# Kernel tuning notes

Measured on AMD Instinct MI355X. Metric: run time of the kernel, lower is better.

The kernel has to match this reference:

```python
import jax, jax.numpy as jnp
import numpy as np

C = 256; C_OUT = 256; HD = 32; NH = 8; WS = 8; SHIFT = WS // 2
B = 2; H = 256; W = 256
HW = H // WS; WW = W // WS; NWIN = HW * WW; P = WS * WS
SCALE = HD ** -0.5
GN_GROUPS = 16; GN_EPS = 1e-5
UP = C // 2; LOW = C - UP; SQ = 2

# relative position index (static)
_ci = np.arange(WS)
_coords = np.stack(np.meshgrid(_ci, _ci, indexing='ij'), -1).reshape(-1, 2)  # [P,2]
_rel = _coords[:, None] - _coords[None, :] + WS - 1                          # [P,P,2]
REL0 = jnp.asarray(_rel[..., 0]); REL1 = jnp.asarray(_rel[..., 1])

# shifted-window mask (static), type != 'W'
_s = WS - SHIFT
_m = np.zeros((HW, WW, WS, WS, WS, WS), bool)
_m[-1, :, :_s, :, _s:, :] = True
_m[-1, :, _s:, :, :_s, :] = True
_m[:, -1, :, :_s, :, _s:] = True
_m[:, -1, :, _s:, :, :_s] = True
MASK = jnp.asarray(_m.reshape(NWIN, P, P))


def to_windows(x):  # [B,H,W,C] -> [B,NWIN,P,C]
    b, h, w, c = x.shape
    return x.reshape(b, h // WS, WS, w // WS, WS, c).transpose(0, 1, 3, 2, 4, 5).reshape(b, NWIN, P, c)


def to_spatial(x):  # [B,NWIN,P,C] -> [B,H,W,C]
    b, _, _, c = x.shape
    return x.reshape(b, HW, WW, WS, WS, c).transpose(0, 1, 3, 2, 4, 5).reshape(b, H, W, c)


def heads(x):  # [B,NWIN,P,C] -> [NH,B,NWIN,P,HD]
    b = x.shape[0]
    return x.reshape(b, NWIN, P, NH, HD).transpose(3, 0, 1, 2, 4)


def conv(x, w, b=None, groups=1, pad=0):
    y = jax.lax.conv_general_dilated(x, w, (1, 1), [(pad, pad), (pad, pad)],
                                     dimension_numbers=('NCHW', 'OIHW', 'NCHW'),
                                     feature_group_count=groups)
    return y if b is None else y + b[None, :, None, None]


def group_norm(x, w, b):  # torch nn.GroupNorm semantics (biased var)
    n, c, h, ww_ = x.shape
    xg = x.reshape(n, GN_GROUPS, -1)
    mu = xg.mean(-1, keepdims=True)
    var = ((xg - mu) ** 2).mean(-1, keepdims=True)
    xg = (xg - mu) / jnp.sqrt(var + GN_EPS)
    return xg.reshape(n, c, h, ww_) * w[None, :, None, None] + b[None, :, None, None]


def sru(x, gn_w, gn_b):
    gn_x = group_norm(x, gn_w, gn_b)
    w_gamma = (gn_w / jnp.sum(gn_w))[None, :, None, None]
    rw = jax.nn.sigmoid(gn_x * w_gamma)
    w1 = jnp.where(rw > 0.5, jnp.ones_like(rw), rw)
    w2 = jnp.where(rw > 0.5, jnp.zeros_like(rw), rw)
    x1 = w1 * x; x2 = w2 * x
    c = x.shape[1] // 2
    return jnp.concatenate([x1[:, :c] + x2[:, c:], x1[:, c:] + x2[:, :c]], axis=1)


def cru(x, sq1_w, sq2_w, gwc_w, gwc_b, pwc1_w, pwc2_w):
    up, low = x[:, :UP], x[:, UP:]
    up = conv(up, sq1_w)          # [B,UP//SQ,H,W]
    low = conv(low, sq2_w)        # [B,LOW//SQ,H,W]
    y1 = conv(up, gwc_w, gwc_b, groups=2, pad=1) + conv(up, pwc1_w)  # [B,C,H,W]
    y2 = jnp.concatenate([conv(low, pwc2_w), low], axis=1)           # [B,C,H,W]
    out = jnp.concatenate([y1, y2], axis=1)                          # [B,2C,H,W]
    pooled = out.mean(axis=(2, 3), keepdims=True)
    out = jax.nn.softmax(pooled, axis=1) * out
    c = out.shape[1] // 2
    return out[:, :c] + out[:, c:]


def setup_inputs():
    key = jax.random.key(0)
    ks = jax.random.split(key, 14)
    r = lambda k, s, sc=1.0: jax.random.normal(k, s, jnp.float32) * sc
    return {
        'x': r(ks[0], (B, C, H, W)),
        'w_qkv': r(ks[1], (3 * C, C), 0.02), 'b_qkv': jnp.zeros((3 * C,), jnp.float32),
        'rel_pos': r(ks[2], (NH, 2 * WS - 1, 2 * WS - 1), 0.02),
        'gn_w': jax.random.uniform(ks[3], (C,), jnp.float32, 0.5, 1.5),
        'gn_b': r(ks[4], (C,), 0.02),
        'sq1_w': r(ks[5], (UP // SQ, UP, 1, 1), 0.05),
        'sq2_w': r(ks[6], (LOW // SQ, LOW, 1, 1), 0.05),
        'gwc_w': r(ks[7], (C, (UP // SQ) // 2, 3, 3), 0.05), 'gwc_b': jnp.zeros((C,), jnp.float32),
        'pwc1_w': r(ks[8], (C, UP // SQ, 1, 1), 0.05),
        'pwc2_w': r(ks[9], (C - LOW // SQ, LOW // SQ, 1, 1), 0.05),
        'w_out': r(ks[10], (C_OUT, C), 0.02), 'b_out': jnp.zeros((C_OUT,), jnp.float32),
    }


def reference(x, w_qkv, b_qkv, rel_pos, gn_w, gn_b, sq1_w, sq2_w, gwc_w, gwc_b, pwc1_w, pwc2_w, w_out, b_out):
    xh = jnp.transpose(x, (0, 2, 3, 1))                       # b h w c
    xh = jnp.roll(xh, (-SHIFT, -SHIFT), axis=(1, 2))          # cyclic shift (type='SW')
    xw = to_windows(xh)                                       # [B,NWIN,P,C]
    qkv = xw @ w_qkv.T + b_qkv                                # [B,NWIN,P,3C]
    # q path: back to spatial -> SRU -> back to windows/heads
    q_sp = jnp.transpose(to_spatial(qkv[..., :C]), (0, 3, 1, 2))
    q_sp = sru(q_sp, gn_w, gn_b)
    q = heads(to_windows(jnp.transpose(q_sp, (0, 2, 3, 1))))  # [NH,B,NWIN,P,HD]
    # k path: CRU
    k_sp = jnp.transpose(to_spatial(qkv[..., C:2 * C]), (0, 3, 1, 2))
    k_sp = cru(k_sp, sq1_w, sq2_w, gwc_w, gwc_b, pwc1_w, pwc2_w)
    k = heads(to_windows(jnp.transpose(k_sp, (0, 2, 3, 1))))
    v = heads(qkv[..., 2 * C:])
    sim = jnp.einsum('hbwpc,hbwqc->hbwpq', q, k) * SCALE
    sim = sim + rel_pos[:, REL0, REL1][:, None, None]         # relative position bias [NH,P,P]
    sim = jnp.where(MASK[None, None], -jnp.inf, sim)
    probs = jax.nn.softmax(sim, axis=-1)
    out = jnp.einsum('hbwpq,hbwqc->hbwpc', probs, v)          # [NH,B,NWIN,P,HD]
    out = jnp.transpose(out, (1, 2, 3, 0, 4)).reshape(B, NWIN, P, C)
    out = out @ w_out.T + b_out
    out = to_spatial(out)                                     # b h w c
    out = jnp.roll(out, (SHIFT, SHIFT), axis=(1, 2))
    return jnp.transpose(out, (0, 3, 1, 2))                   # b c h w
```

## Files before the change

kernel.cpp:

```cpp
#include <hip/hip_runtime.h>
#include <hip/hip_bf16.h>

typedef __hip_bfloat16 bf16;
typedef __attribute__((ext_vector_type(8))) short s16x8;
typedef __attribute__((ext_vector_type(4))) float f32x4;

#define SCALE 0.17677669529663687f

#define OFF_QKV   0ull
#define OFF_UL    201326592ull
#define OFF_CRU   268435456ull
#define OFF_XT    OFF_CRU
#define OFF_POOL  402653184ull
#define OFF_GNACC 402657280ull
#define OFF_GNFIN 402657536ull
#define OFF_SOFT  402658048ull
#define OFF_WC    402662144ull
#define OFF_WC2   403022592ull
#define OFF_WQS   403088128ull
#define OFF_WOS   403481344ull
#define OFF_ATTN  OFF_UL

__device__ __forceinline__ float b2f(bf16 v){ return __bfloat162float(v); }
__device__ __forceinline__ bf16  f2b(float v){ return __float2bfloat16(v); }
__device__ __forceinline__ ushort f2bu(float v){ bf16 b = __float2bfloat16(v); return *(ushort*)&b; }
__device__ __forceinline__ uint pk2(float a, float b){ return (uint)f2bu(a) | ((uint)f2bu(b) << 16); }

__device__ __forceinline__ void gload16(const void* g, void* l){
  __builtin_amdgcn_global_load_lds((const __attribute__((address_space(1))) unsigned int*)g,
                                   (__attribute__((address_space(3))) unsigned int*)l, 16, 0, 0);
}

__global__ void k_wprep(const float* __restrict__ gwc_w, const float* __restrict__ pwc1,
                        const float* __restrict__ pwc2, const float* __restrict__ w_qkv,
                        const float* __restrict__ w_out, float* __restrict__ Wc,
                        float* __restrict__ Wc2, char* __restrict__ wqs, char* __restrict__ wos)
{
  int idx = blockIdx.x * 256 + threadIdx.x;
  if (idx < 90112){
    int c = idx & 127;
    int gk = idx >> 7;
    int g = gk / 352, k = gk - g * 352;
    int ch = g * 128 + c;
    Wc[idx] = (k < 288) ? gwc_w[(size_t)ch * 288 + k] : pwc1[ch * 64 + (k - 288)];
  } else if (idx < 106496){
    int j = idx - 90112;
    int k = j >> 8, c = j & 255;
    Wc2[j] = (c < 192) ? pwc2[c * 64 + k] : (k == (c - 192) ? 1.f : 0.f);
  } else if (idx < 303104){
    int j = idx - 106496;
    int n = j >> 8, k = j & 255;
    *(ushort*)(wqs + (size_t)n * 512 + ((k * 2) ^ ((n & 7) << 4))) = f2bu(w_qkv[n * 256 + k]);
  } else if (idx < 368640){
    int j = idx - 303104;
    int n = j >> 8, k = j & 255;
    *(ushort*)(wos + (size_t)n * 512 + ((k * 2) ^ ((n & 7) << 4))) = f2bu(w_out[n * 256 + k]);
  }
}

__global__ __launch_bounds__(256) void k_xt(const float* __restrict__ x, char* __restrict__ xt)
{
  __shared__ ushort Ls[64][66];
  int t = threadIdx.x;
  int jt = blockIdx.x;
  int i  = blockIdx.y;
  int zc = blockIdx.z;
  int ct = zc & 3, b = zc >> 2;
  int ch0 = ct * 64, j0 = jt * 64;
  for (int e = t; e < 4096; e += 256){
    int ch = e >> 6, jj = e & 63;
    Ls[ch][jj] = f2bu(x[(((size_t)(b * 256 + ch0 + ch)) << 16) + (i << 8) + j0 + jj]);
  }
  __syncthreads();
  int ri = (i - 4) & 255;
  #pragma unroll
  for (int s = 0; s < 2; s++){
    int id = s * 256 + t;
    int jj = id >> 3, blk = id & 7;
    int rj = (j0 + jj - 4) & 255;
    int m = (b << 16) + (ri << 8) + rj;
    ushort u0 = Ls[blk*8+0][jj], u1 = Ls[blk*8+1][jj], u2 = Ls[blk*8+2][jj], u3 = Ls[blk*8+3][jj];
    ushort u4 = Ls[blk*8+4][jj], u5 = Ls[blk*8+5][jj], u6 = Ls[blk*8+6][jj], u7 = Ls[blk*8+7][jj];
    uint4 pkv;
    pkv.x = (uint)u0 | ((uint)u1 << 16);
    pkv.y = (uint)u2 | ((uint)u3 << 16);
    pkv.z = (uint)u4 | ((uint)u5 << 16);
    pkv.w = (uint)u6 | ((uint)u7 << 16);
    size_t byte = (size_t)m * 512 + (((ch0 + blk * 8) * 2) ^ ((m & 7) << 4));
    *(uint4*)(xt + byte) = pkv;
  }
}

__global__ __launch_bounds__(256) void k_qkv_mfma(
    const char* __restrict__ xt, const char* __restrict__ wq,
    const float* __restrict__ bias, bf16* __restrict__ qkv)
{
  __shared__ char sm[32768];
  int t = threadIdx.x;
  int l = t & 63, w = t >> 6;
  int ln = l & 15, l4 = l >> 4;
  int m0 = blockIdx.x * 128, n0 = blockIdx.y * 128;
  int wm0 = (w >> 1) * 64, wn0 = (w & 1) * 64;
  f32x4 acc[4][4];
  #pragma unroll
  for (int a = 0; a < 4; a++)
    #pragma unroll
    for (int c = 0; c < 4; c++) acc[a][c] = (f32x4){0.f, 0.f, 0.f, 0.f};
  const char* gA = xt + (size_t)(m0 + w * 32 + (l >> 3)) * 512 + (l & 7) * 16;
  const char* gB = wq + (size_t)(n0 + w * 32 + (l >> 3)) * 512 + (l & 7) * 16;
  char* ldsA = sm + (w * 32) * 128;
  char* ldsB = sm + 16384 + (w * 32) * 128;
  for (int k0 = 0; k0 < 256; k0 += 64){
    #pragma unroll
    for (int c = 0; c < 4; c++){
      gload16(gA + (size_t)k0 * 2 + c * 4096, ldsA + c * 1024);
      gload16(gB + (size_t)k0 * 2 + c * 4096, ldsB + c * 1024);
    }
    __syncthreads();
    s16x8 af[4][2], bfr[4][2];
    #pragma unroll
    for (int mi = 0; mi < 4; mi++){
      int r = wm0 + mi * 16 + ln;
      int key = (r & 7) << 4;
      #pragma unroll
      for (int kk = 0; kk < 2; kk++)
        af[mi][kk] = *(const s16x8*)(sm + r * 128 + ((kk * 64 + l4 * 16) ^ key));
    }
    #pragma unroll
    for (int ni = 0; ni < 4; ni++){
      int r = wn0 + ni * 16 + ln;
      int key = (r & 7) << 4;
      #pragma unroll
      for (int kk = 0; kk < 2; kk++)
        bfr[ni][kk] = *(const s16x8*)(sm + 16384 + r * 128 + ((kk * 64 + l4 * 16) ^ key));
    }
    #pragma unroll
    for (int kk = 0; kk < 2; kk++)
      #pragma unroll
      for (int mi = 0; mi < 4; mi++)
        #pragma unroll
        for (int ni = 0; ni < 4; ni++)
          acc[mi][ni] = __builtin_amdgcn_mfma_f32_16x16x32_bf16(af[mi][kk], bfr[ni][kk], acc[mi][ni], 0, 0, 0);
    __syncthreads();
  }
  #pragma unroll
  for (int ni = 0; ni < 4; ni++){
    int n = n0 + wn0 + ni * 16 + ln;
    float bs = bias[n];
    #pragma unroll
    for (int mi = 0; mi < 4; mi++){
      int mb = m0 + wm0 + mi * 16 + l4 * 4;
      int b = mb >> 16, pix = mb & 65535;
      ushort4 pkv;
      pkv.x = f2bu(acc[mi][ni].x + bs);
      pkv.y = f2bu(acc[mi][ni].y + bs);
      pkv.z = f2bu(acc[mi][ni].z + bs);
      pkv.w = f2bu(acc[mi][ni].w + bs);
      *(ushort4*)((char*)qkv + (((size_t)(b * 768 + n)) << 17) + pix * 2) = pkv;
    }
  }
}

__global__ __launch_bounds__(256) void k_gn_stats(const bf16* __restrict__ qkv,
                                                  float* __restrict__ acc)
{
  int blk = blockIdx.x;
  int s = blk & 7, bg = blk >> 3;
  int g = bg & 15, b = bg >> 4;
  int t = threadIdx.x;
  float sum = 0.f, sq = 0.f;
  for (int ch = 0; ch < 16; ch++){
    const bf16* base = qkv + (((size_t)(b * 768 + g * 16 + ch)) << 16) + s * 8192;
    for (int p = t; p < 8192; p += 256){
      float v = b2f(base[p]);
      sum += v; sq += v * v;
    }
  }
  __shared__ float rs[256], rq[256];
  rs[t] = sum; rq[t] = sq; __syncthreads();
  for (int st = 128; st > 0; st >>= 1){
    if (t < st){ rs[t] += rs[t + st]; rq[t] += rq[t + st]; }
    __syncthreads();
  }
  if (t == 0){
    atomicAdd(&acc[bg * 2], rs[0]);
    atomicAdd(&acc[bg * 2 + 1], rq[0]);
  }
}

__global__ __launch_bounds__(256) void k_gn_final(const float* __restrict__ acc,
                                                  const float* __restrict__ gn_w,
                                                  float* __restrict__ fin)
{
  __shared__ float red[256];
  int t = threadIdx.x;
  red[t] = gn_w[t]; __syncthreads();
  for (int st = 128; st > 0; st >>= 1){
    if (t < st) red[t] += red[t + st];
    __syncthreads();
  }
  if (t == 0) fin[64] = 1.0f / red[0];
  if (t < 32){
    const float Ninv = 1.0f / 1048576.0f;
    float mu = acc[t * 2] * Ninv;
    float var = acc[t * 2 + 1] * Ninv - mu * mu;
    fin[t * 2] = mu;
    fin[t * 2 + 1] = 1.0f / sqrtf(var + 1e-5f);
  }
}

__global__ __launch_bounds__(256) void k_sru(bf16* __restrict__ qkv,
    const float* __restrict__ fin, const float* __restrict__ gn_w,
    const float* __restrict__ gn_b)
{
  int idx = blockIdx.x * 256 + threadIdx.x;
  int pix = idx & 65535;
  int bc = idx >> 16;
  int c = bc & 127, b = bc >> 7;
  size_t i1 = (((size_t)(b * 768 + c)) << 16) + pix;
  size_t i2 = (((size_t)(b * 768 + c + 128)) << 16) + pix;
  float x1 = b2f(qkv[i1]);
  float x2 = b2f(qkv[i2]);
  int g1 = c >> 4, g2 = (c + 128) >> 4;
  float mu1 = fin[(b * 16 + g1) * 2], rs1 = fin[(b * 16 + g1) * 2 + 1];
  float mu2 = fin[(b * 16 + g2) * 2], rs2 = fin[(b * 16 + g2) * 2 + 1];
  float invs = fin[64];
  float w1c = gn_w[c], w2c = gn_w[c + 128];
  float gnx1 = (x1 - mu1) * rs1 * w1c + gn_b[c];
  float gnx2 = (x2 - mu2) * rs2 * w2c + gn_b[c + 128];
  float rw1 = 1.0f / (1.0f + __expf(-gnx1 * (w1c * invs)));
  float rw2 = 1.0f / (1.0f + __expf(-gnx2 * (w2c * invs)));
  float a1 = rw1 > 0.5f ? 1.0f : rw1, a2 = rw1 > 0.5f ? 0.0f : rw1;
  float b1 = rw2 > 0.5f ? 1.0f : rw2, b2v = rw2 > 0.5f ? 0.0f : rw2;
  qkv[i1] = f2b(a1 * x1 + b2v * x2);
  qkv[i2] = f2b(b1 * x2 + a2 * x1);
}

__global__ __launch_bounds__(256) void k_squeeze(const bf16* __restrict__ qkv,
    const float* __restrict__ sq1, const float* __restrict__ sq2,
    float* __restrict__ ul)
{
  __shared__ float in_s[128][65];
  int p0 = blockIdx.x * 64;
  int b = p0 >> 16, pl0 = p0 & 65535;
  int t = threadIdx.x;
  int pp = t & 63, og = t >> 6;
  for (int e = t; e < 8192; e += 256){
    int ch = e >> 6, px = e & 63;
    in_s[ch][px] = b2f(qkv[(((size_t)(b * 768 + 256 + ch)) << 16) + pl0 + px]);
  }
  __syncthreads();
  {
    float acc[16] = {};
    for (int i = 0; i < 128; i++){
      float v = in_s[i][pp];
      #pragma unroll
      for (int o = 0; o < 16; o++) acc[o] += sq1[(og * 16 + o) * 128 + i] * v;
    }
    #pragma unroll
    for (int o = 0; o < 16; o++)
      ul[(((size_t)(b * 128 + og * 16 + o)) << 16) + pl0 + pp] = acc[o];
  }
  __syncthreads();
  for (int e = t; e < 8192; e += 256){
    int ch = e >> 6, px = e & 63;
    in_s[ch][px] = b2f(qkv[(((size_t)(b * 768 + 384 + ch)) << 16) + pl0 + px]);
  }
  __syncthreads();
  {
    float acc[16] = {};
    for (int i = 0; i < 128; i++){
      float v = in_s[i][pp];
      #pragma unroll
      for (int o = 0; o < 16; o++) acc[o] += sq2[(og * 16 + o) * 128 + i] * v;
    }
    #pragma unroll
    for (int o = 0; o < 16; o++)
      ul[(((size_t)(b * 128 + 64 + og * 16 + o)) << 16) + pl0 + pp] = acc[o];
  }
}

__global__ __launch_bounds__(256) void k_cru_gemm(
    const float* __restrict__ ul, const float* __restrict__ Wmat,
    const float* __restrict__ gwc_b, bf16* __restrict__ cru, int mode)
{
  __shared__ float As[16][132];
  __shared__ float Bs[16][132];
  int t = threadIdx.x;
  int tx = t & 15, ty = t >> 4;
  int tile = blockIdx.x;
  int yT = blockIdx.y;
  int b = blockIdx.z;
  int tr = tile >> 4, tc = tile & 15;
  int ty0 = tr * 8, tx0 = tc * 16;
  int K = (mode == 0) ? 352 : 64;
  const float* W = (mode == 0) ? (Wmat + yT * 352 * 128) : Wmat;
  int wstride = (mode == 0) ? 128 : 256;
  int wcol0 = (mode == 0) ? 0 : yT * 128;
  float acc[8][8] = {};
  for (int k0 = 0; k0 < K; k0 += 16){
    #pragma unroll
    for (int l = 0; l < 8; l++){
      int e = t + l * 256;
      int mm = e & 127, kk = e >> 7;
      int k = k0 + kk;
      int py = mm >> 4, pxx = mm & 15;
      float v;
      if (mode == 0){
        int i, dy, dx;
        if (k < 288){
          i = k / 9; int r9 = k - i * 9; dy = r9 / 3; dx = r9 - dy * 3;
          i += yT * 32;
        } else { i = k - 288; dy = 1; dx = 1; }
        int gy = ty0 + py + dy - 1, gx = tx0 + pxx + dx - 1;
        v = (gy >= 0 && gy < 256 && gx >= 0 && gx < 256)
              ? ul[(((size_t)(b * 128 + i)) << 16) + (gy << 8) + gx] : 0.f;
      } else {
        v = ul[(((size_t)(b * 128 + 64 + k)) << 16) + ((ty0 + py) << 8) + tx0 + pxx];
      }
      As[kk][mm] = v;
    }
    #pragma unroll
    for (int l = 0; l < 8; l++){
      int e = t + l * 256;
      int nn = e & 127, kk = e >> 7;
      Bs[kk][nn] = W[(size_t)(k0 + kk) * wstride + wcol0 + nn];
    }
    __syncthreads();
    #pragma unroll
    for (int kk = 0; kk < 16; kk++){
      float4 a0 = *(const float4*)&As[kk][ty * 4];
      float4 a1 = *(const float4*)&As[kk][64 + ty * 4];
      float4 b0 = *(const float4*)&Bs[kk][tx * 4];
      float4 b1 = *(const float4*)&Bs[kk][64 + tx * 4];
      float av[8] = {a0.x,a0.y,a0.z,a0.w,a1.x,a1.y,a1.z,a1.w};
      float bv[8] = {b0.x,b0.y,b0.z,b0.w,b1.x,b1.y,b1.z,b1.w};
      #pragma unroll
      for (int r = 0; r < 8; r++)
        #pragma unroll
        for (int c = 0; c < 8; c++) acc[r][c] += av[r] * bv[c];
    }
    __syncthreads();
  }
  #pragma unroll
  for (int r = 0; r < 8; r++){
    int mr = (r < 4) ? (ty * 4 + r) : (64 + ty * 4 + r - 4);
    int py = mr >> 4, pxx = mr & 15;
    int gpix = ((ty0 + py) << 8) + tx0 + pxx;
    #pragma unroll
    for (int c = 0; c < 8; c++){
      int nc = (c < 4) ? (tx * 4 + c) : (64 + tx * 4 + c - 4);
      int ch; float bv;
      if (mode == 0){ ch = yT * 128 + nc; bv = gwc_b[ch]; }
      else          { ch = 256 + yT * 128 + nc; bv = 0.f; }
      cru[(((size_t)(b * 512 + ch)) << 16) + gpix] = f2b(acc[r][c] + bv);
    }
  }
}

__global__ __launch_bounds__(256) void k_pool(const bf16* __restrict__ cru,
                                              float* __restrict__ pool)
{
  int bc = blockIdx.x;
  const ushort4* p4 = (const ushort4*)(cru + (((size_t)bc) << 16));
  int t = threadIdx.x;
  float s = 0.f;
  for (int i = t; i < 16384; i += 256){
    ushort4 u = p4[i];
    s += b2f(*(bf16*)&u.x) + b2f(*(bf16*)&u.y) + b2f(*(bf16*)&u.z) + b2f(*(bf16*)&u.w);
  }
  __shared__ float red[256];
  red[t] = s; __syncthreads();
  for (int st = 128; st > 0; st >>= 1){
    if (t < st) red[t] += red[t + st];
    __syncthreads();
  }
  if (t == 0) pool[bc] = red[0];
}

__global__ __launch_bounds__(512) void k_pool_softmax(const float* __restrict__ pool,
                                                      float* __restrict__ s)
{
  __shared__ float red[512];
  int t = threadIdx.x;
  for (int b = 0; b < 2; b++){
    float v = pool[b * 512 + t] * (1.0f / 65536.0f);
    red[t] = v; __syncthreads();
    for (int st = 256; st > 0; st >>= 1){
      if (t < st) red[t] = fmaxf(red[t], red[t + st]);
      __syncthreads();
    }
    float m = red[0]; __syncthreads();
    float e = __expf(v - m);
    red[t] = e; __syncthreads();
    for (int st = 256; st > 0; st >>= 1){
      if (t < st) red[t] += red[t + st];
      __syncthreads();
    }
    float inv = 1.0f / red[0];
    __syncthreads();
    s[b * 512 + t] = e * inv;
  }
}

__global__ __launch_bounds__(256) void k_cru_apply(const bf16* __restrict__ cru,
    const float* __restrict__ s, bf16* __restrict__ qkv)
{
  int idx = blockIdx.x * 256 + threadIdx.x;
  int pix = idx & 65535;
  int bc = idx >> 16;
  int c = bc & 255, b = bc >> 8;
  float v1 = b2f(cru[(((size_t)(b * 512 + c)) << 16) + pix]);
  float v2 = b2f(cru[(((size_t)(b * 512 + 256 + c)) << 16) + pix]);
  float kv = s[b * 512 + c] * v1 + s[b * 512 + 256 + c] * v2;
  qkv[(((size_t)(b * 768 + 256 + c)) << 16) + pix] = f2b(kv);
}

__global__ __launch_bounds__(64) void k_attn(const bf16* __restrict__ qkv,
    const float* __restrict__ rel_pos, char* __restrict__ attnb)
{
  __shared__ float k_s[64][33];
  __shared__ float v_s[64][33];
  __shared__ float bias_s[225];
  int win = blockIdx.x, head = blockIdx.y, b = blockIdx.z;
  int hw = win >> 5, wwi = win & 31;
  int t = threadIdx.x;
  for (int e = t; e < 225; e += 64) bias_s[e] = rel_pos[head * 225 + e];
  int pi = t >> 3, pj = t & 7;
  int pix = ((hw * 8 + pi) << 8) | (wwi * 8 + pj);
  size_t base = ((size_t)(b * 768)) << 16;
  float q[32];
  #pragma unroll
  for (int d = 0; d < 32; d++){
    q[d]      = b2f(qkv[base + (((size_t)(      head * 32 + d)) << 16) + pix]);
    k_s[t][d] = b2f(qkv[base + (((size_t)(256 + head * 32 + d)) << 16) + pix]);
    v_s[t][d] = b2f(qkv[base + (((size_t)(512 + head * 32 + d)) << 16) + pix]);
  }
  __syncthreads();
  bool mH = (hw == 31), mW = (wwi == 31);
  float sim[64];
  float mx = -1e30f;
  #pragma unroll
  for (int j = 0; j < 64; j++){
    float sv = 0.f;
    #pragma unroll
    for (int d = 0; d < 32; d++) sv += q[d] * k_s[j][d];
    int ji = j >> 3, jj = j & 7;
    sv = sv * SCALE + bias_s[(pi - ji + 7) * 15 + (pj - jj + 7)];
    bool masked = (mH && ((pi < 4) != (ji < 4))) || (mW && ((pj < 4) != (jj < 4)));
    sv = masked ? -1e30f : sv;
    sim[j] = sv;
    mx = fmaxf(mx, sv);
  }
  float sum = 0.f;
  #pragma unroll
  for (int j = 0; j < 64; j++){
    float e = __expf(sim[j] - mx);
    sim[j] = e; sum += e;
  }
  float inv = 1.0f / sum;
  float o[32] = {};
  #pragma unroll
  for (int j = 0; j < 64; j++){
    float p = sim[j] * inv;
    #pragma unroll
    for (int d = 0; d < 32; d++) o[d] += p * v_s[j][d];
  }
  int ii = hw * 8 + pi, jjp = wwi * 8 + pj;
  int om = (b << 16) + (((ii + 4) & 255) << 8) + ((jjp + 4) & 255);
  size_t rb = (size_t)om * 512;
  int key = (om & 7) << 4;
  #pragma unroll
  for (int d0 = 0; d0 < 32; d0 += 8){
    uint4 pkv;
    pkv.x = pk2(o[d0+0], o[d0+1]);
    pkv.y = pk2(o[d0+2], o[d0+3]);
    pkv.z = pk2(o[d0+4], o[d0+5]);
    pkv.w = pk2(o[d0+6], o[d0+7]);
    *(uint4*)(attnb + rb + ((head * 64 + d0 * 2) ^ key)) = pkv;
  }
}

__global__ __launch_bounds__(256) void k_proj_mfma(
    const char* __restrict__ at, const char* __restrict__ wo,
    const float* __restrict__ bias, float* __restrict__ outp)
{
  __shared__ char sm[32768];
  int t = threadIdx.x;
  int l = t & 63, w = t >> 6;
  int ln = l & 15, l4 = l >> 4;
  int m0 = blockIdx.x * 128, n0 = blockIdx.y * 128;
  int wm0 = (w >> 1) * 64, wn0 = (w & 1) * 64;
  f32x4 acc[4][4];
  #pragma unroll
  for (int a = 0; a < 4; a++)
    #pragma unroll
    for (int c = 0; c < 4; c++) acc[a][c] = (f32x4){0.f, 0.f, 0.f, 0.f};
  const char* gA = at + (size_t)(m0 + w * 32 + (l >> 3)) * 512 + (l & 7) * 16;
  const char* gB = wo + (size_t)(n0 + w * 32 + (l >> 3)) * 512 + (l & 7) * 16;
  char* ldsA = sm + (w * 32) * 128;
  char* ldsB = sm + 16384 + (w * 32) * 128;
  for (int k0 = 0; k0 < 256; k0 += 64){
    #pragma unroll
    for (int c = 0; c < 4; c++){
      gload16(gA + (size_t)k0 * 2 + c * 4096, ldsA + c * 1024);
      gload16(gB + (size_t)k0 * 2 + c * 4096, ldsB + c * 1024);
    }
    __syncthreads();
    s16x8 af[4][2], bfr[4][2];
    #pragma unroll
    for (int mi = 0; mi < 4; mi++){
      int r = wm0 + mi * 16 + ln;
      int key = (r & 7) << 4;
      #pragma unroll
      for (int kk = 0; kk < 2; kk++)
        af[mi][kk] = *(const s16x8*)(sm + r * 128 + ((kk * 64 + l4 * 16) ^ key));
    }
    #pragma unroll
    for (int ni = 0; ni < 4; ni++){
      int r = wn0 + ni * 16 + ln;
      int key = (r & 7) << 4;
      #pragma unroll
      for (int kk = 0; kk < 2; kk++)
        bfr[ni][kk] = *(const s16x8*)(sm + 16384 + r * 128 + ((kk * 64 + l4 * 16) ^ key));
    }
    #pragma unroll
    for (int kk = 0; kk < 2; kk++)
      #pragma unroll
      for (int mi = 0; mi < 4; mi++)
        #pragma unroll
        for (int ni = 0; ni < 4; ni++)
          acc[mi][ni] = __builtin_amdgcn_mfma_f32_16x16x32_bf16(af[mi][kk], bfr[ni][kk], acc[mi][ni], 0, 0, 0);
    __syncthreads();
  }
  #pragma unroll
  for (int ni = 0; ni < 4; ni++){
    int n = n0 + wn0 + ni * 16 + ln;
    float bs = bias[n];
    #pragma unroll
    for (int mi = 0; mi < 4; mi++){
      int mb = m0 + wm0 + mi * 16 + l4 * 4;
      int b = mb >> 16, pix = mb & 65535;
      float4 v;
      v.x = acc[mi][ni].x + bs;
      v.y = acc[mi][ni].y + bs;
      v.z = acc[mi][ni].z + bs;
      v.w = acc[mi][ni].w + bs;
      *(float4*)(outp + (((size_t)(b * 256 + n)) << 16) + pix) = v;
    }
  }
}

extern "C" void kernel_launch(void* const* d_in, const int* in_sizes, int n_in,
                              void* d_out, int out_size, void* d_ws, size_t ws_size,
                              hipStream_t stream) {
  const float* x       = (const float*)d_in[0];
  const float* w_qkv   = (const float*)d_in[1];
  const float* b_qkv   = (const float*)d_in[2];
  const float* rel_pos = (const float*)d_in[3];
  const float* gn_w    = (const float*)d_in[4];
  const float* gn_b    = (const float*)d_in[5];
  const float* sq1     = (const float*)d_in[6];
  const float* sq2     = (const float*)d_in[7];
  const float* gwc_w   = (const float*)d_in[8];
  const float* gwc_b   = (const float*)d_in[9];
  const float* pwc1    = (const float*)d_in[10];
  const float* pwc2    = (const float*)d_in[11];
  const float* w_out   = (const float*)d_in[12];
  const float* b_out   = (const float*)d_in[13];
  float* out = (float*)d_out;

  char* ws = (char*)d_ws;
  bf16*  qkv   = (bf16*)(ws + OFF_QKV);
  float* ul    = (float*)(ws + OFF_UL);
  bf16*  cru   = (bf16*)(ws + OFF_CRU);
  char*  xt    = ws + OFF_XT;
  float* pool  = (float*)(ws + OFF_POOL);
  float* gnacc = (float*)(ws + OFF_GNACC);
  float* gnfin = (float*)(ws + OFF_GNFIN);
  float* smax  = (float*)(ws + OFF_SOFT);
  float* Wc    = (float*)(ws + OFF_WC);
  float* Wc2   = (float*)(ws + OFF_WC2);
  char*  wqs   = ws + OFF_WQS;
  char*  wos   = ws + OFF_WOS;
  char*  attnb = ws + OFF_ATTN;

  hipMemsetAsync(ws + OFF_GNACC, 0, 256, stream);
  k_wprep<<<1440, 256, 0, stream>>>(gwc_w, pwc1, pwc2, w_qkv, w_out, Wc, Wc2, wqs, wos);
  k_xt<<<dim3(4, 256, 8), 256, 0, stream>>>(x, xt);
  k_qkv_mfma<<<dim3(1024, 6), 256, 0, stream>>>(xt, wqs, b_qkv, qkv);
  k_gn_stats<<<256, 256, 0, stream>>>(qkv, gnacc);
  k_gn_final<<<1, 256, 0, stream>>>(gnacc, gn_w, gnfin);
  k_sru<<<65536, 256, 0, stream>>>(qkv, gnfin, gn_w, gn_b);
  k_squeeze<<<2048, 256, 0, stream>>>(qkv, sq1, sq2, ul);
  k_cru_gemm<<<dim3(512, 2, 2), 256, 0, stream>>>(ul, Wc, gwc_b, cru, 0);
  k_cru_gemm<<<dim3(512, 2, 2), 256, 0, stream>>>(ul, Wc2, gwc_b, cru, 1);
  k_pool<<<1024, 256, 0, stream>>>(cru, pool);
  k_pool_softmax<<<1, 512, 0, stream>>>(pool, smax);
  k_cru_apply<<<131072, 256, 0, stream>>>(cru, smax, qkv);
  k_attn<<<dim3(1024, 8, 2), 64, 0, stream>>>(qkv, rel_pos, attnb);
  k_proj_mfma<<<dim3(1024, 2), 256, 0, stream>>>(attnb, wos, b_out, out);
}
```

Baseline: 2.529 ms.

## Process four adjacent windows per attention block for coalesced loads and reused LDS

The attention kernel now runs 256-thread blocks that each cover four horizontally adjacent windows, so a wavefront reads 32 contiguous pixels per channel plane instead of 8. This gives better-coalesced global loads. K and V share a single float4-vectorized LDS buffer, with V loaded after the softmax, which lowers LDS use and permits three blocks per CU under the launch bounds. The cost is an extra barrier, partial unrolling of the inner loops, and more register pressure.

```diff
diff --git a/kernel.cpp b/kernel.cpp
--- a/kernel.cpp
+++ b/kernel.cpp
@@ -416,58 +416,95 @@
   qkv[(((size_t)(b * 768 + 256 + c)) << 16) + pix] = f2b(kv);
 }
 
-__global__ __launch_bounds__(64) void k_attn(const bf16* __restrict__ qkv,
+__global__ __launch_bounds__(256, 3) void k_attn(const bf16* __restrict__ qkv,
     const float* __restrict__ rel_pos, char* __restrict__ attnb)
 {
-  __shared__ float k_s[64][33];
-  __shared__ float v_s[64][33];
+  __shared__ float kv_s[64 * 4 * 36];
   __shared__ float bias_s[225];
-  int win = blockIdx.x, head = blockIdx.y, b = blockIdx.z;
-  int hw = win >> 5, wwi = win & 31;
-  int t = threadIdx.x;
-  for (int e = t; e < 225; e += 64) bias_s[e] = rel_pos[head * 225 + e];
-  int pi = t >> 3, pj = t & 7;
-  int pix = ((hw * 8 + pi) << 8) | (wwi * 8 + pj);
+  int t = threadIdx.x;
+  int wg = blockIdx.x, hw = blockIdx.y;
+  int z = blockIdx.z;
+  int head = z & 7, b = z >> 3;
+  int r = t >> 5, c = t & 31;
+  int win = c >> 3, pj = c & 7, pi = r;
+  int i = hw * 8 + r, j = wg * 32 + c;
+  int pix = (i << 8) | j;
+  int jpix = r * 8 + pj;
+  int lrow = ((jpix << 2) | win) * 36;
   size_t base = ((size_t)(b * 768)) << 16;
+  int h32 = head * 32;
+
+  for (int e = t; e < 225; e += 256) bias_s[e] = rel_pos[head * 225 + e];
+
   float q[32];
   #pragma unroll
-  for (int d = 0; d < 32; d++){
-    q[d]      = b2f(qkv[base + (((size_t)(      head * 32 + d)) << 16) + pix]);
-    k_s[t][d] = b2f(qkv[base + (((size_t)(256 + head * 32 + d)) << 16) + pix]);
-    v_s[t][d] = b2f(qkv[base + (((size_t)(512 + head * 32 + d)) << 16) + pix]);
+  for (int d4 = 0; d4 < 8; d4++){
+    float kv0 = b2f(qkv[base + (((size_t)(256 + h32 + d4*4+0)) << 16) + pix]);
+    float kv1 = b2f(qkv[base + (((size_t)(256 + h32 + d4*4+1)) << 16) + pix]);
+    float kv2 = b2f(qkv[base + (((size_t)(256 + h32 + d4*4+2)) << 16) + pix]);
+    float kv3 = b2f(qkv[base + (((size_t)(256 + h32 + d4*4+3)) << 16) + pix]);
+    *(float4*)&kv_s[lrow + d4*4] = make_float4(kv0, kv1, kv2, kv3);
+    q[d4*4+0] = b2f(qkv[base + (((size_t)(h32 + d4*4+0)) << 16) + pix]);
+    q[d4*4+1] = b2f(qkv[base + (((size_t)(h32 + d4*4+1)) << 16) + pix]);
+    q[d4*4+2] = b2f(qkv[base + (((size_t)(h32 + d4*4+2)) << 16) + pix]);
+    q[d4*4+3] = b2f(qkv[base + (((size_t)(h32 + d4*4+3)) << 16) + pix]);
   }
   __syncthreads();
-  bool mH = (hw == 31), mW = (wwi == 31);
+
+  bool mH = (hw == 31), mW = (wg == 7 && win == 3);
   float sim[64];
   float mx = -1e30f;
-  #pragma unroll
-  for (int j = 0; j < 64; j++){
+  #pragma unroll 4
+  for (int jp = 0; jp < 64; jp++){
+    const float4* kp = (const float4*)&kv_s[((jp << 2) | win) * 36];
     float sv = 0.f;
     #pragma unroll
-    for (int d = 0; d < 32; d++) sv += q[d] * k_s[j][d];
-    int ji = j >> 3, jj = j & 7;
+    for (int d4 = 0; d4 < 8; d4++){
+      float4 kk = kp[d4];
+      sv += q[d4*4+0]*kk.x + q[d4*4+1]*kk.y + q[d4*4+2]*kk.z + q[d4*4+3]*kk.w;
+    }
+    int ji = jp >> 3, jj = jp & 7;
     sv = sv * SCALE + bias_s[(pi - ji + 7) * 15 + (pj - jj + 7)];
     bool masked = (mH && ((pi < 4) != (ji < 4))) || (mW && ((pj < 4) != (jj < 4)));
     sv = masked ? -1e30f : sv;
-    sim[j] = sv;
+    sim[jp] = sv;
     mx = fmaxf(mx, sv);
   }
   float sum = 0.f;
   #pragma unroll
-  for (int j = 0; j < 64; j++){
-    float e = __expf(sim[j] - mx);
-    sim[j] = e; sum += e;
+  for (int jp = 0; jp < 64; jp++){
+    float e = __expf(sim[jp] - mx);
+    sim[jp] = e; sum += e;
   }
   float inv = 1.0f / sum;
+  __syncthreads();
+
+  #pragma unroll
+  for (int d4 = 0; d4 < 8; d4++){
+    float v0 = b2f(qkv[base + (((size_t)(512 + h32 + d4*4+0)) << 16) + pix]);
+    float v1 = b2f(qkv[base + (((size_t)(512 + h32 + d4*4+1)) << 16) + pix]);
+    float v2 = b2f(qkv[base + (((size_t)(512 + h32 + d4*4+2)) << 16) + pix]);
+    float v3 = b2f(qkv[base + (((size_t)(512 + h32 + d4*4+3)) << 16) + pix]);
+    *(float4*)&kv_s[lrow + d4*4] = make_float4(v0, v1, v2, v3);
+  }
+  __syncthreads();
+
   float o[32] = {};
-  #pragma unroll
-  for (int j = 0; j < 64; j++){
-    float p = sim[j] * inv;
-    #pragma unroll
-    for (int d = 0; d < 32; d++) o[d] += p * v_s[j][d];
-  }
-  int ii = hw * 8 + pi, jjp = wwi * 8 + pj;
-  int om = (b << 16) + (((ii + 4) & 255) << 8) + ((jjp + 4) & 255);
+  #pragma unroll 4
+  for (int jp = 0; jp < 64; jp++){
+    float p = sim[jp] * inv;
+    const float4* vp = (const float4*)&kv_s[((jp << 2) | win) * 36];
+    #pragma unroll
+    for (int d4 = 0; d4 < 8; d4++){
+      float4 vv = vp[d4];
+      o[d4*4+0] += p * vv.x;
+      o[d4*4+1] += p * vv.y;
+      o[d4*4+2] += p * vv.z;
+      o[d4*4+3] += p * vv.w;
+    }
+  }
+
+  int om = (b << 16) + (((i + 4) & 255) << 8) + ((j + 4) & 255);
   size_t rb = (size_t)om * 512;
   int key = (om & 7) << 4;
   #pragma unroll
@@ -598,6 +635,6 @@
   k_pool<<<1024, 256, 0, stream>>>(cru, pool);
   k_pool_softmax<<<1, 512, 0, stream>>>(pool, smax);
   k_cru_apply<<<131072, 256, 0, stream>>>(cru, smax, qkv);
-  k_attn<<<dim3(1024, 8, 2), 64, 0, stream>>>(qkv, rel_pos, attnb);
+  k_attn<<<dim3(8, 32, 16), 256, 0, stream>>>(qkv, rel_pos, attnb);
   k_proj_mfma<<<dim3(1024, 2), 256, 0, stream>>>(attnb, wos, b_out, out);
 }
```

Measured after the change: 2.197 ms. -13.1%, faster.
